# Kernel tuning notes

Hardware: AMD Instinct MI355X
Metric: run time of the kernel (lower is better)

Reference implementation:

```python
import jax, jax.numpy as jnp
import numpy as np

LAYERS, BLOCKS = 10, 3
N_BLK = LAYERS * BLOCKS
RC, SC, K = 128, 128, 2
IN_CH, COND_CH, OUT_CH = 256, 80, 256
DILATIONS = tuple(2 ** (i % LAYERS) for i in range(N_BLK))
INV_SQRT2 = 0.70710678118


def conv1x1(x, w, b):
    # x: [B, I, T], w: [O, I], b: [O] -> [B, O, T]
    return jnp.einsum('oi,bit->bot', w, x) + b[None, :, None]


def causal_conv(x, w, b, dilation):
    # x: [B, C, T], w: [O, I, K]; left-pad by (K-1)*d == torch pad-both + right slice
    pad = (w.shape[2] - 1) * dilation
    y = jax.lax.conv_general_dilated(
        x, w, window_strides=(1,), padding=[(pad, 0)],
        rhs_dilation=(dilation,), dimension_numbers=('NCH', 'OIH', 'NCH'))
    return y + b[None, :, None]


def setup_inputs() -> dict:
    key = jax.random.key(0)
    ks = jax.random.split(key, 20)
    s = 0.05
    B, T = 2, 8000
    inp = {
        'x': jax.random.normal(ks[0], (B, IN_CH, T), jnp.float32),
        'condition': jax.random.normal(ks[1], (B, COND_CH, T), jnp.float32),
        'input_w': jax.random.normal(ks[2], (RC, IN_CH), jnp.float32) * s,
        'input_b': jax.random.normal(ks[3], (RC,), jnp.float32) * s,
        'dil_w': jax.random.normal(ks[4], (N_BLK, RC, RC, K), jnp.float32) * s,
        'dil_b': jax.random.normal(ks[5], (N_BLK, RC), jnp.float32) * s,
        'gate_w': jax.random.normal(ks[6], (N_BLK, RC, RC), jnp.float32) * s,
        'gate_b': jax.random.normal(ks[7], (N_BLK, RC), jnp.float32) * s,
        'cond_w': jax.random.normal(ks[8], (N_BLK, RC, COND_CH), jnp.float32) * s,
        'cond_b': jax.random.normal(ks[9], (N_BLK, RC), jnp.float32) * s,
        'condg_w': jax.random.normal(ks[10], (N_BLK, RC, COND_CH), jnp.float32) * s,
        'condg_b': jax.random.normal(ks[11], (N_BLK, RC), jnp.float32) * s,
        'res_w': jax.random.normal(ks[12], (N_BLK, RC, RC), jnp.float32) * s,
        'res_b': jax.random.normal(ks[13], (N_BLK, RC), jnp.float32) * s,
        'skip_w': jax.random.normal(ks[14], (N_BLK, SC, RC), jnp.float32) * s,
        'skip_b': jax.random.normal(ks[15], (N_BLK, SC), jnp.float32) * s,
        'out1_w': jax.random.normal(ks[16], (SC, SC), jnp.float32) * s,
        'out1_b': jax.random.normal(ks[17], (SC,), jnp.float32) * s,
        'out2_w': jax.random.normal(ks[18], (OUT_CH, SC), jnp.float32) * s,
        'out2_b': jax.random.normal(ks[19], (OUT_CH,), jnp.float32) * s,
    }
    return inp


def reference(x, condition, input_w, input_b, dil_w, dil_b, gate_w, gate_b,
              cond_w, cond_b, condg_w, condg_b, res_w, res_b,
              skip_w, skip_b, out1_w, out1_b, out2_w, out2_b):
    h = conv1x1(x, input_w, input_b)  # [B, RC, T]
    skip = jnp.zeros_like(conv1x1(h, skip_w[0], skip_b[0]) * 0)  # [B, SC, T]
    for i, d in enumerate(DILATIONS):
        a = causal_conv(h, dil_w[i], dil_b[i], d) + conv1x1(condition, cond_w[i], cond_b[i])
        g = conv1x1(h, gate_w[i], gate_b[i]) + conv1x1(condition, condg_w[i], condg_b[i])
        out = jnp.tanh(a) * jax.nn.sigmoid(g)
        h = (h + conv1x1(out, res_w[i], res_b[i])) * INV_SQRT2
        skip = skip + conv1x1(out, skip_w[i], skip_b[i])
    y = jax.nn.relu(conv1x1(skip, out1_w, out1_b))
    return conv1x1(y, out2_w, out2_b)  # [B, 256, T]
```

## Files before the change

### kernel.cpp

```cpp
#include <hip/hip_runtime.h>

#define T_LEN 8000
#define NTPB 125
#define NBLK 250
#define NLAYER 30
#define GUARD 512
#define HROWS (GUARD + T_LEN)
#define SLAB (HROWS * 128)
#define INV_SQRT2 0.70710678118f

typedef short bf16x8 __attribute__((ext_vector_type(8)));
typedef unsigned uint2v __attribute__((ext_vector_type(2)));
typedef unsigned uint4v __attribute__((ext_vector_type(4)));
typedef float f32x4 __attribute__((ext_vector_type(4)));

#define R_HT  0
#define R_OUT 8192
#define R_CND 16384
#define WBASE 22528
#define LDS_SHORTS 71680

#define KLINE 4096
#define LS 106496
#define C1 16384
#define C2 32768
#define C3 49152
#define C4 57344
#define C5 73728
#define C6 90112
#define IN_OFF   3194880
#define OUT1_OFF 3227648
#define OUT2_OFF 3244032

#define WAITV(N) asm volatile("s_waitcnt vmcnt(" #N ")" ::: "memory")
#define LGKM0    asm volatile("s_waitcnt lgkmcnt(0)" ::: "memory")
#define BAR      asm volatile("s_barrier" ::: "memory")

__device__ __forceinline__ unsigned short f2bf_u(float f) {
    union { float f; unsigned u; } v; v.f = f;
    unsigned u = v.u + 0x7FFFu + ((v.u >> 16) & 1u);
    return (unsigned short)(u >> 16);
}
__device__ __forceinline__ short f2bf(float f) { return (short)f2bf_u(f); }

__device__ __forceinline__ unsigned cvtpk(float lo, float hi) {
    unsigned r;
    asm("v_cvt_pk_bf16_f32 %0, %1, %2" : "=v"(r) : "v"(lo), "v"(hi));
    return r;
}

__device__ __forceinline__ float gated_act(float av, float gv) {
    float e  = __expf(-2.f * fabsf(av));
    float th = (1.f - e) * __builtin_amdgcn_rcpf(1.f + e);
    th = (av < 0.f) ? -th : th;
    float sg = __builtin_amdgcn_rcpf(1.f + __expf(-gv));
    return th * sg;
}

__device__ __forceinline__ void ldg16_sc1(bf16x8* d, const short* p) {
    asm volatile("global_load_dwordx4 %0, %1, off sc1" : "=v"(*d) : "v"(p));
}
__device__ __forceinline__ void stg8_sc1(short* p, uint2v v) {
    asm volatile("global_store_dwordx2 %0, %1, off sc1" : : "v"(p), "v"(v) : "memory");
}
__device__ __forceinline__ void st_flag(int* p, int v) {
    __hip_atomic_store(p, v, __ATOMIC_RELAXED, __HIP_MEMORY_SCOPE_AGENT);
}
__device__ __forceinline__ void wait_ge(const int* p, int v) {
    while (__hip_atomic_load(p, __ATOMIC_RELAXED, __HIP_MEMORY_SCOPE_AGENT) < v)
        __builtin_amdgcn_s_sleep(1);
}

__device__ __forceinline__ f32x4 mfma_(bf16x8 a, bf16x8 b, f32x4 c) {
    return __builtin_amdgcn_mfma_f32_16x16x32_bf16(a, b, c, 0, 0, 0);
}

__device__ __forceinline__ void gload_lds16(const short* g, short* l) {
    __builtin_amdgcn_global_load_lds(
        (const __attribute__((address_space(1))) unsigned int*)g,
        (__attribute__((address_space(3))) unsigned int*)l, 16, 0, 0);
}
__device__ __forceinline__ void stageW2(const short* src, short* dst, int wv, int lane) {
    gload_lds16(src + wv * 512 + lane * 8, dst + wv * 512);
    gload_lds16(src + (16 + wv) * 512 + lane * 8, dst + (16 + wv) * 512);
}
__device__ __forceinline__ void stageW1(const short* src, short* dst, int wv, int lane) {
    gload_lds16(src + wv * 512 + lane * 8, dst + wv * 512);
}

template<int NP>
__device__ __forceinline__ void pairN(const short* wb, const short* sm, int boff,
                                      int ks0, int lg, int awoff,
                                      f32x4* ac0, f32x4* ac1)
{
#pragma unroll
    for (int p = 0; p < NP; ++p) {
        bf16x8 B = *(const bf16x8*)&sm[boff + ((ks0 + p) * 4 + lg) * 512];
#pragma unroll
        for (int mt = 0; mt < 2; ++mt) {
            bf16x8 a0 = *(const bf16x8*)&wb[p * 8192 + awoff + mt * 512];
            ac0[mt] = mfma_(a0, B, ac0[mt]);
            bf16x8 a1 = *(const bf16x8*)&wb[p * 8192 + 4096 + awoff + mt * 512];
            ac1[mt] = mfma_(a1, B, ac1[mt]);
        }
    }
}
template<int NP>
__device__ __forceinline__ void singleN(const short* wb, const short* sm, int boff,
                                        int ks0, int lg, int awoff, f32x4* ac)
{
#pragma unroll
    for (int p = 0; p < NP; ++p) {
        bf16x8 B = *(const bf16x8*)&sm[boff + ((ks0 + p) * 4 + lg) * 512];
#pragma unroll
        for (int mt = 0; mt < 2; ++mt) {
            bf16x8 a = *(const bf16x8*)&wb[p * 4096 + awoff + mt * 512];
            ac[mt] = mfma_(a, B, ac[mt]);
        }
    }
}

__global__ __launch_bounds__(256) void k_pack(
    const float* __restrict__ dil_w, const float* __restrict__ gate_w,
    const float* __restrict__ cond_w, const float* __restrict__ condg_w,
    const float* __restrict__ res_w, const float* __restrict__ skip_w,
    const float* __restrict__ input_w, const float* __restrict__ out1_w,
    const float* __restrict__ out2_w,
    const float* __restrict__ dil_b, const float* __restrict__ cond_b,
    const float* __restrict__ gate_b, const float* __restrict__ condg_b,
    short* __restrict__ wp, short* __restrict__ hbt, int* __restrict__ flg)
{
    int gid = blockIdx.x * 256 + threadIdx.x;
    if (gid < 512) flg[gid] = 0;
    {
        int g2 = gid - 512;
        if (g2 >= 0 && g2 < 262144) {
            unsigned* hb32 = (unsigned*)hbt;
            int slab = g2 >> 15, off = g2 & 32767;
            hb32[(size_t)slab * (SLAB / 2) + off] = 0u;
        }
    }
    if (gid >= 6400 * 64) return;
    int fid = gid >> 6, lane = gid & 63;
    int lr = lane & 15, lg = lane >> 4;
    float v[8];
    if (fid < 6240) {
        int layer = fid / 208;
        int r = fid - layer * 208;
        int kl = r >> 3, f = r & 7;
        int m = f * 16 + lr;
        size_t mi = (size_t)layer * 128 + m;
        int mat, ks;
        if      (kl < 8)  { mat = (kl & 1) ? 2 : 1; ks = kl >> 1; }
        else if (kl < 14) { mat = (kl & 1) ? 4 : 3; ks = (kl - 8) >> 1; }
        else if (kl < 18) { mat = 0; ks = kl - 14; }
        else              { mat = (kl & 1) ? 6 : 5; ks = (kl - 18) >> 1; }
        int kb = ks * 32 + lg * 8;
#pragma unroll
        for (int e = 0; e < 8; ++e) {
            int k = kb + e;
            float val;
            switch (mat) {
                case 0:  val = dil_w[(mi * 128 + k) * 2];     break;
                case 1:  val = dil_w[(mi * 128 + k) * 2 + 1]; break;
                case 2:  val = gate_w[mi * 128 + k]; break;
                case 3:  val = (k < 80) ? cond_w[mi * 80 + k]
                               : ((k == 80) ? dil_b[mi] + cond_b[mi] : 0.f); break;
                case 4:  val = (k < 80) ? condg_w[mi * 80 + k]
                               : ((k == 80) ? gate_b[mi] + condg_b[mi] : 0.f); break;
                case 5:  val = res_w[mi * 128 + k]; break;
                default: val = skip_w[mi * 128 + k]; break;
            }
            v[e] = val;
        }
    } else if (fid < 6304) {
        int f = fid - 6240; int ks = f >> 3, fr = f & 7;
        int m = fr * 16 + lr; int kb = ks * 32 + lg * 8;
#pragma unroll
        for (int e = 0; e < 8; ++e) v[e] = input_w[(size_t)m * 256 + kb + e];
    } else if (fid < 6336) {
        int f = fid - 6304; int ks = f >> 3, fr = f & 7;
        int m = fr * 16 + lr; int kb = ks * 32 + lg * 8;
#pragma unroll
        for (int e = 0; e < 8; ++e) v[e] = out1_w[(size_t)m * 128 + kb + e];
    } else {
        int f = fid - 6336; int mt = f & 15; int ks = f >> 4;
        int m = mt * 16 + lr; int kb = ks * 32 + lg * 8;
#pragma unroll
        for (int e = 0; e < 8; ++e) v[e] = out2_w[(size_t)m * 128 + kb + e];
    }
    short* dst = wp + (size_t)fid * 512 + lane * 8;
#pragma unroll
    for (int e = 0; e < 8; ++e) dst[e] = f2bf(v[e]);
}

__global__ __launch_bounds__(1024, 4) void k_wavenet(
    const float* __restrict__ x, const float* __restrict__ cond,
    const short* __restrict__ wp, short* __restrict__ hbt,
    const float* __restrict__ ib, const float* __restrict__ rbias,
    const float* __restrict__ sbias, const float* __restrict__ b1,
    const float* __restrict__ b2, float* __restrict__ outp,
    int* __restrict__ rdy, int* __restrict__ dn)
{
    __shared__ __align__(16) short sm[LDS_SHORTS];

    const int tid  = threadIdx.x;
    const int lane = tid & 63;
    const int wv   = __builtin_amdgcn_readfirstlane(tid >> 6);
    const int wm   = wv & 3;
    const int wn   = wv >> 2;
    const int lr   = lane & 15, lg = lane >> 4;
    const int bidx = blockIdx.x;
    const int b    = bidx / NTPB;
    const int ti   = bidx - b * NTPB;
    const int t0   = ti * 64;
    const int tl   = wn * 16 + lr;
    const int tg   = t0 + tl;
    const int tl8  = tl * 8;
    const int lane8 = lane * 8;
    const int awoff = wm * 1024 + lane8;
    const int chA  = wm * 32 + lg * 4;
    const int kbA  = wm * 4 + (lg >> 1);
    const int e0   = (lg & 1) * 4;

    stageW2(wp + IN_OFF, (short*)&sm[WBASE], wv, lane);
    stageW2(wp + IN_OFF + 16384, (short*)&sm[WBASE + 16384], wv, lane);
    {
        const float* xb = x + (size_t)b * 256 * T_LEN + t0 + lane;
#pragma unroll
        for (int it = 0; it < 2; ++it) {
            int kb = wv * 2 + it;
            unsigned pk[4];
#pragma unroll
            for (int e = 0; e < 4; ++e)
                pk[e] = cvtpk(xb[(size_t)(kb * 8 + 2 * e) * T_LEN],
                              xb[(size_t)(kb * 8 + 2 * e + 1) * T_LEN]);
            *(uint4v*)&sm[(kb * 64 + lane) * 8] = *(uint4v*)pk;
        }
        if (wv < 12) {
            const float* cb = cond + (size_t)b * 80 * T_LEN + t0 + lane;
            unsigned pk[4];
#pragma unroll
            for (int e = 0; e < 4; ++e) {
                int c0 = wv * 8 + 2 * e, c1 = c0 + 1;
                float v0 = (c0 < 80) ? cb[(size_t)c0 * T_LEN] : ((c0 == 80) ? 1.f : 0.f);
                float v1 = (c1 < 80) ? cb[(size_t)c1 * T_LEN] : 0.f;
                pk[e] = cvtpk(v0, v1);
            }
            *(uint4v*)&sm[R_CND + (wv * 64 + lane) * 8] = *(uint4v*)pk;
        }
    }
    __syncthreads();

    f32x4 hres[2] = {{0.f,0.f,0.f,0.f},{0.f,0.f,0.f,0.f}};
    {
        f32x4 acc[2] = {{0.f,0.f,0.f,0.f},{0.f,0.f,0.f,0.f}};
        singleN<4>((const short*)&sm[WBASE], sm, tl8, 0, lg, awoff, acc);
        singleN<4>((const short*)&sm[WBASE + 16384], sm, tl8, 4, lg, awoff, acc);
#pragma unroll
        for (int mt = 0; mt < 2; ++mt) {
            int cb0 = chA + mt * 16;
            f32x4 bv = {ib[cb0], ib[cb0 + 1], ib[cb0 + 2], ib[cb0 + 3]};
            hres[mt] = acc[mt] + bv;
        }
    }
    __syncthreads();
    {
        short* hrow = hbt + (size_t)b * SLAB + (size_t)(GUARD + tg) * 128 + chA;
#pragma unroll
        for (int mt = 0; mt < 2; ++mt) {
            uint2v hv = {cvtpk(hres[mt][0], hres[mt][1]), cvtpk(hres[mt][2], hres[mt][3])};
            stg8_sc1(hrow + mt * 16, hv);
            *(uint2v*)&sm[R_HT + ((kbA + mt * 2) * 64 + tl) * 8 + e0] = hv;
        }
    }
    asm volatile("s_waitcnt vmcnt(0)" ::: "memory");
    __syncthreads();
    if (tid == 0) st_flag(&rdy[bidx], 1);

    f32x4 skp[2] = {{0.f,0.f,0.f,0.f},{0.f,0.f,0.f,0.f}};

    int rot = 0;
    for (int li = 0; li < NLAYER; ++li) {
        const int d   = 1 << (li % 10);
        const int ksh = (d + 63) >> 6;
        const short* wl  = wp + (size_t)li * LS;
        const short* hcb = hbt + (size_t)((li & 3) * 2 + b) * SLAB;
        short*       hnb = hbt + (size_t)(((li + 1) & 3) * 2 + b) * SLAB;
        const int rA = rot;
        const int rB = (rot + 1) % 3;
        const int rC = (rot + 2) % 3;
        short* const sA = (short*)&sm[WBASE + rA * 16384];
        short* const sB = (short*)&sm[WBASE + rB * 16384];
        short* const sC = (short*)&sm[WBASE + rC * 16384];

        if (lane == 0 && ti >= ksh) wait_ge(&rdy[bidx - ksh], li + 1);

        f32x4 rbv[2], sbv[2];
        {
            const float* rbl = rbias + li * 128 + chA;
            const float* sbl = sbias + li * 128 + chA;
#pragma unroll
            for (int mt = 0; mt < 2; ++mt) {
                rbv[mt] = (f32x4){rbl[mt*16], rbl[mt*16+1], rbl[mt*16+2], rbl[mt*16+3]};
                sbv[mt] = (f32x4){sbl[mt*16], sbl[mt*16+1], sbl[mt*16+2], sbl[mt*16+3]};
            }
        }

        stageW2(wl, sA, wv, lane);
        bf16x8 Bg[4];
        {
            const short* hr = hcb + (size_t)(GUARD + tg - d) * 128 + lg * 8;
#pragma unroll
            for (int ks = 0; ks < 4; ++ks) ldg16_sc1(&Bg[ks], hr + ks * 32);
        }
        stageW2(wl + C1, sB, wv, lane);
        stageW2(wl + C2, sC, wv, lane);

        WAITV(8); BAR;
        f32x4 aa[2] = {{0.f,0.f,0.f,0.f},{0.f,0.f,0.f,0.f}};
        f32x4 ag[2] = {{0.f,0.f,0.f,0.f},{0.f,0.f,0.f,0.f}};
        pairN<2>(sA, sm, R_HT + tl8, 0, lg, awoff, aa, ag);

        WAITV(2); BAR;
        if (tid == 0) st_flag(&dn[bidx], li + 1);
        stageW1(wl + C3, sA, wv, lane);
        pairN<2>(sB, sm, R_HT + tl8, 2, lg, awoff, aa, ag);

        WAITV(1); BAR;
        stageW2(wl + C4, sB, wv, lane);
        pairN<2>(sC, sm, R_CND + tl8, 0, lg, awoff, aa, ag);

        WAITV(2); BAR;
        stageW2(wl + C5, sC, wv, lane);
        pairN<1>(sA, sm, R_CND + tl8, 2, lg, awoff, aa, ag);

        WAITV(2); BAR;
        stageW2(wl + C6, sA, wv, lane);
        {
#pragma unroll
            for (int ks = 0; ks < 4; ++ks) {
#pragma unroll
                for (int mt = 0; mt < 2; ++mt) {
                    bf16x8 a = *(const bf16x8*)&sB[ks * 4096 + awoff + mt * 512];
                    aa[mt] = mfma_(a, Bg[ks], aa[mt]);
                }
            }
        }
#pragma unroll
        for (int mt = 0; mt < 2; ++mt) {
            uint2v ov = {cvtpk(gated_act(aa[mt][0], ag[mt][0]), gated_act(aa[mt][1], ag[mt][1])),
                         cvtpk(gated_act(aa[mt][2], ag[mt][2]), gated_act(aa[mt][3], ag[mt][3]))};
            *(uint2v*)&sm[R_OUT + ((kbA + mt * 2) * 64 + tl) * 8 + e0] = ov;
        }
        WAITV(2); LGKM0; BAR;

        f32x4 ar[2]  = {{0.f,0.f,0.f,0.f},{0.f,0.f,0.f,0.f}};
        f32x4 as2[2] = {{0.f,0.f,0.f,0.f},{0.f,0.f,0.f,0.f}};
        pairN<2>(sC, sm, R_OUT + tl8, 0, lg, awoff, ar, as2);
        if (lane == 0 && li >= 3) {
            int d3 = 1 << ((li - 3) % 10);
            int k3 = (d3 + 63) >> 6;
            if (ti + k3 < NTPB) wait_ge(&dn[bidx + k3], li - 2);
        }
        WAITV(0); BAR;
        pairN<2>(sA, sm, R_OUT + tl8, 2, lg, awoff, ar, as2);

#pragma unroll
        for (int mt = 0; mt < 2; ++mt) {
            skp[mt]  = skp[mt] + as2[mt] + sbv[mt];
            hres[mt] = (hres[mt] + ar[mt] + rbv[mt]) * INV_SQRT2;
        }
        if (li < NLAYER - 1) {
            short* hrow = hnb + (size_t)(GUARD + tg) * 128 + chA;
#pragma unroll
            for (int mt = 0; mt < 2; ++mt) {
                uint2v hv = {cvtpk(hres[mt][0], hres[mt][1]), cvtpk(hres[mt][2], hres[mt][3])};
                stg8_sc1(hrow + mt * 16, hv);
                *(uint2v*)&sm[R_HT + ((kbA + mt * 2) * 64 + tl) * 8 + e0] = hv;
            }
        }
        WAITV(0); LGKM0; BAR;
        if (tid == 0 && li < NLAYER - 1) st_flag(&rdy[bidx], li + 2);
        rot = (rot + 1) % 3;
    }

    stageW2(wp + OUT1_OFF, (short*)&sm[WBASE], wv, lane);
    stageW2(wp + OUT2_OFF, (short*)&sm[WBASE + 16384], wv, lane);
    stageW2(wp + OUT2_OFF + 16384, (short*)&sm[WBASE + 32768], wv, lane);
#pragma unroll
    for (int mt = 0; mt < 2; ++mt) {
        uint2v sv = {cvtpk(skp[mt][0], skp[mt][1]), cvtpk(skp[mt][2], skp[mt][3])};
        *(uint2v*)&sm[R_HT + ((kbA + mt * 2) * 64 + tl) * 8 + e0] = sv;
    }
    __syncthreads();
    f32x4 ay[2] = {{0.f,0.f,0.f,0.f},{0.f,0.f,0.f,0.f}};
    singleN<4>((const short*)&sm[WBASE], sm, R_HT + tl8, 0, lg, awoff, ay);
#pragma unroll
    for (int mt = 0; mt < 2; ++mt) {
        int cb0 = chA + mt * 16;
        float y0 = fmaxf(ay[mt][0] + b1[cb0],     0.f);
        float y1 = fmaxf(ay[mt][1] + b1[cb0 + 1], 0.f);
        float y2 = fmaxf(ay[mt][2] + b1[cb0 + 2], 0.f);
        float y3 = fmaxf(ay[mt][3] + b1[cb0 + 3], 0.f);
        uint2v yv = {cvtpk(y0, y1), cvtpk(y2, y3)};
        *(uint2v*)&sm[R_OUT + ((kbA + mt * 2) * 64 + tl) * 8 + e0] = yv;
    }
    __syncthreads();
    f32x4 ao[4] = {{0.f,0.f,0.f,0.f},{0.f,0.f,0.f,0.f},
                   {0.f,0.f,0.f,0.f},{0.f,0.f,0.f,0.f}};
    {
        const short* w2a = (const short*)&sm[WBASE + 16384];
        const short* w2b = (const short*)&sm[WBASE + 32768];
#pragma unroll
        for (int ksp = 0; ksp < 2; ++ksp) {
            bf16x8 B = *(const bf16x8*)&sm[R_OUT + tl8 + (ksp * 4 + lg) * 512];
#pragma unroll
            for (int mt = 0; mt < 4; ++mt) {
                int fg = 4 * wm + mt;
                bf16x8 A = *(const bf16x8*)&w2a[(ksp * 2 + (fg >> 3)) * 4096 + (fg & 7) * 512 + lane8];
                ao[mt] = mfma_(A, B, ao[mt]);
            }
        }
#pragma unroll
        for (int ksp = 0; ksp < 2; ++ksp) {
            bf16x8 B = *(const bf16x8*)&sm[R_OUT + tl8 + ((2 + ksp) * 4 + lg) * 512];
#pragma unroll
            for (int mt = 0; mt < 4; ++mt) {
                int fg = 4 * wm + mt;
                bf16x8 A = *(const bf16x8*)&w2b[(ksp * 2 + (fg >> 3)) * 4096 + (fg & 7) * 512 + lane8];
                ao[mt] = mfma_(A, B, ao[mt]);
            }
        }
    }
#pragma unroll
    for (int mt = 0; mt < 4; ++mt) {
        int ch2 = wm * 64 + mt * 16 + lg * 4;
        float* op = outp + ((size_t)(b * 256 + ch2)) * T_LEN + tg;
        op[0]         = ao[mt][0] + b2[ch2];
        op[T_LEN]     = ao[mt][1] + b2[ch2 + 1];
        op[2 * T_LEN] = ao[mt][2] + b2[ch2 + 2];
        op[3 * T_LEN] = ao[mt][3] + b2[ch2 + 3];
    }
}

extern "C" void kernel_launch(void* const* d_in, const int* in_sizes, int n_in,
                              void* d_out, int out_size, void* d_ws, size_t ws_size,
                              hipStream_t stream)
{
    const float* x       = (const float*)d_in[0];
    const float* cond    = (const float*)d_in[1];
    const float* input_w = (const float*)d_in[2];
    const float* input_b = (const float*)d_in[3];
    const float* dil_w   = (const float*)d_in[4];
    const float* dil_b   = (const float*)d_in[5];
    const float* gate_w  = (const float*)d_in[6];
    const float* gate_b  = (const float*)d_in[7];
    const float* cond_w  = (const float*)d_in[8];
    const float* cond_b  = (const float*)d_in[9];
    const float* condg_w = (const float*)d_in[10];
    const float* condg_b = (const float*)d_in[11];
    const float* res_w   = (const float*)d_in[12];
    const float* res_b   = (const float*)d_in[13];
    const float* skip_w  = (const float*)d_in[14];
    const float* skip_b  = (const float*)d_in[15];
    const float* out1_w  = (const float*)d_in[16];
    const float* out1_b  = (const float*)d_in[17];
    const float* out2_w  = (const float*)d_in[18];
    const float* out2_b  = (const float*)d_in[19];
    float* outp = (float*)d_out;

    short* wpk = (short*)d_ws;
    short* hbt = wpk + (size_t)6400 * 512;
    int*   flg = (int*)(hbt + (size_t)8 * SLAB);
    int*   rdy = flg;
    int*   dn  = flg + 256;

    k_pack<<<1600, 256, 0, stream>>>(dil_w, gate_w, cond_w, condg_w, res_w, skip_w,
                                     input_w, out1_w, out2_w,
                                     dil_b, cond_b, gate_b, condg_b, wpk, hbt, flg);

    void* args[] = {(void*)&x, (void*)&cond, (void*)&wpk, (void*)&hbt,
                    (void*)&input_b, (void*)&res_b, (void*)&skip_b,
                    (void*)&out1_b, (void*)&out2_b, (void*)&outp,
                    (void*)&rdy, (void*)&dn};
    (void)hipLaunchCooperativeKernel((void*)k_wavenet, dim3(NBLK), dim3(1024), args, 0, stream);
}
```

Measured before the change: 328.4 us.

## Warp-specialize producer/consumer waves and deepen the h-buffer ring

Splits the 16 waves into 8 consumer waves that run all MFMA work (each handling two time sub-tiles) and 8 producer waves that stage weights into LDS and fetch the dilated h tile into a new LDS region. The ring of h buffers grows from 4 to 6 levels, and the global h layout changes from row-major with a guard to tiled slabs. This relaxes the cross-block dn dependency and moves the flag waits onto producer waves. The aim is to overlap global loads and inter-block waits with compute and cut the consumers' exposed latency. In exchange, compute is concentrated on half the waves, LDS use grows, and workspace footprint increases.

```diff
diff --git a/kernel.cpp b/kernel.cpp
--- a/kernel.cpp
+++ b/kernel.cpp
@@ -4,12 +4,14 @@
 #define NTPB 125
 #define NBLK 250
 #define NLAYER 30
-#define GUARD 512
-#define HROWS (GUARD + T_LEN)
-#define SLAB (HROWS * 128)
+#define NLVL 6
+#define GTILES 8
+#define TILES_ALL (GTILES + NTPB)
+#define SLAB ((size_t)TILES_ALL * 8192)
 #define INV_SQRT2 0.70710678118f
 
 typedef short bf16x8 __attribute__((ext_vector_type(8)));
+typedef short s16x4  __attribute__((ext_vector_type(4)));
 typedef unsigned uint2v __attribute__((ext_vector_type(2)));
 typedef unsigned uint4v __attribute__((ext_vector_type(4)));
 typedef float f32x4 __attribute__((ext_vector_type(4)));
@@ -17,10 +19,10 @@
 #define R_HT  0
 #define R_OUT 8192
 #define R_CND 16384
-#define WBASE 22528
-#define LDS_SHORTS 71680
-
-#define KLINE 4096
+#define R_HD  22528
+#define WBASE 30720
+#define LDS_SHORTS 79872
+
 #define LS 106496
 #define C1 16384
 #define C2 32768
@@ -42,13 +44,15 @@
     return (unsigned short)(u >> 16);
 }
 __device__ __forceinline__ short f2bf(float f) { return (short)f2bf_u(f); }
-
+__device__ __forceinline__ float bf2f(short s) {
+    union { unsigned u; float f; } v; v.u = ((unsigned)(unsigned short)s) << 16;
+    return v.f;
+}
 __device__ __forceinline__ unsigned cvtpk(float lo, float hi) {
     unsigned r;
     asm("v_cvt_pk_bf16_f32 %0, %1, %2" : "=v"(r) : "v"(lo), "v"(hi));
     return r;
 }
-
 __device__ __forceinline__ float gated_act(float av, float gv) {
     float e  = __expf(-2.f * fabsf(av));
     float th = (1.f - e) * __builtin_amdgcn_rcpf(1.f + e);
@@ -56,7 +60,6 @@
     float sg = __builtin_amdgcn_rcpf(1.f + __expf(-gv));
     return th * sg;
 }
-
 __device__ __forceinline__ void ldg16_sc1(bf16x8* d, const short* p) {
     asm volatile("global_load_dwordx4 %0, %1, off sc1" : "=v"(*d) : "v"(p));
 }
@@ -70,11 +73,9 @@
     while (__hip_atomic_load(p, __ATOMIC_RELAXED, __HIP_MEMORY_SCOPE_AGENT) < v)
         __builtin_amdgcn_s_sleep(1);
 }
-
 __device__ __forceinline__ f32x4 mfma_(bf16x8 a, bf16x8 b, f32x4 c) {
     return __builtin_amdgcn_mfma_f32_16x16x32_bf16(a, b, c, 0, 0, 0);
 }
-
 __device__ __forceinline__ void gload_lds16(const short* g, short* l) {
     __builtin_amdgcn_global_load_lds(
         (const __attribute__((address_space(1))) unsigned int*)g,
@@ -84,24 +85,56 @@
     gload_lds16(src + wv * 512 + lane * 8, dst + wv * 512);
     gload_lds16(src + (16 + wv) * 512 + lane * 8, dst + (16 + wv) * 512);
 }
-__device__ __forceinline__ void stageW1(const short* src, short* dst, int wv, int lane) {
-    gload_lds16(src + wv * 512 + lane * 8, dst + wv * 512);
+__device__ __forceinline__ void stageP4(const short* src, short* dst, int pv, int lane) {
+#pragma unroll
+    for (int r = 0; r < 4; ++r) {
+        int o = (r * 8 + pv) * 64;
+        gload_lds16(src + (o + lane) * 8, dst + o * 8);
+    }
+}
+__device__ __forceinline__ void stageP2(const short* src, short* dst, int pv, int lane) {
+#pragma unroll
+    for (int r = 0; r < 2; ++r) {
+        int o = (r * 8 + pv) * 64;
+        gload_lds16(src + (o + lane) * 8, dst + o * 8);
+    }
 }
 
 template<int NP>
-__device__ __forceinline__ void pairN(const short* wb, const short* sm, int boff,
-                                      int ks0, int lg, int awoff,
-                                      f32x4* ac0, f32x4* ac1)
+__device__ __forceinline__ void pair2t(const short* wb, const short* sm, int reg,
+                                       int tc0, int tc1, int ks0, int lg, int awoff,
+                                       f32x4 (&A)[2][2], f32x4 (&G)[2][2])
 {
 #pragma unroll
     for (int p = 0; p < NP; ++p) {
-        bf16x8 B = *(const bf16x8*)&sm[boff + ((ks0 + p) * 4 + lg) * 512];
+        int slot = reg + ((ks0 + p) * 4 + lg) * 512;
+        bf16x8 B0 = *(const bf16x8*)&sm[slot + tc0 * 8];
+        bf16x8 B1 = *(const bf16x8*)&sm[slot + tc1 * 8];
 #pragma unroll
         for (int mt = 0; mt < 2; ++mt) {
             bf16x8 a0 = *(const bf16x8*)&wb[p * 8192 + awoff + mt * 512];
-            ac0[mt] = mfma_(a0, B, ac0[mt]);
+            A[mt][0] = mfma_(a0, B0, A[mt][0]);
+            A[mt][1] = mfma_(a0, B1, A[mt][1]);
             bf16x8 a1 = *(const bf16x8*)&wb[p * 8192 + 4096 + awoff + mt * 512];
-            ac1[mt] = mfma_(a1, B, ac1[mt]);
+            G[mt][0] = mfma_(a1, B0, G[mt][0]);
+            G[mt][1] = mfma_(a1, B1, G[mt][1]);
+        }
+    }
+}
+__device__ __forceinline__ void d0gemm(const short* wb, const short* sm, int reg,
+                                       int tc0, int tc1, int lg, int awoff,
+                                       f32x4 (&A)[2][2])
+{
+#pragma unroll
+    for (int ks = 0; ks < 4; ++ks) {
+        int slot = reg + (ks * 4 + lg) * 512;
+        bf16x8 B0 = *(const bf16x8*)&sm[slot + tc0 * 8];
+        bf16x8 B1 = *(const bf16x8*)&sm[slot + tc1 * 8];
+#pragma unroll
+        for (int mt = 0; mt < 2; ++mt) {
+            bf16x8 a = *(const bf16x8*)&wb[ks * 4096 + awoff + mt * 512];
+            A[mt][0] = mfma_(a, B0, A[mt][0]);
+            A[mt][1] = mfma_(a, B1, A[mt][1]);
         }
     }
 }
@@ -134,7 +167,7 @@
     if (gid < 512) flg[gid] = 0;
     {
         int g2 = gid - 512;
-        if (g2 >= 0 && g2 < 262144) {
+        if (g2 >= 0 && g2 < 393216) {
             unsigned* hb32 = (unsigned*)hbt;
             int slab = g2 >> 15, off = g2 & 32767;
             hb32[(size_t)slab * (SLAB / 2) + off] = 0u;
@@ -208,23 +241,34 @@
     const int lane = tid & 63;
     const int wv   = __builtin_amdgcn_readfirstlane(tid >> 6);
     const int wm   = wv & 3;
-    const int wn   = wv >> 2;
+    const int wn4  = wv >> 2;
     const int lr   = lane & 15, lg = lane >> 4;
     const int bidx = blockIdx.x;
     const int b    = bidx / NTPB;
     const int ti   = bidx - b * NTPB;
     const int t0   = ti * 64;
-    const int tl   = wn * 16 + lr;
-    const int tg   = t0 + tl;
-    const int tl8  = tl * 8;
+    const int tl4  = wn4 * 16 + lr;
+    const int tg4  = t0 + tl4;
+    const int tl8  = tl4 * 8;
     const int lane8 = lane * 8;
     const int awoff = wm * 1024 + lane8;
     const int chA  = wm * 32 + lg * 4;
     const int kbA  = wm * 4 + (lg >> 1);
     const int e0   = (lg & 1) * 4;
-
-    stageW2(wp + IN_OFF, (short*)&sm[WBASE], wv, lane);
-    stageW2(wp + IN_OFF + 16384, (short*)&sm[WBASE + 16384], wv, lane);
+    const bool cons = (wv < 8);
+    const int pv   = wv - 8;
+    const int wn2  = wn4 & 1;
+    const int tc0  = wn2 * 32 + lr;
+    const int tc1  = tc0 + 16;
+    const int tgc0 = t0 + tc0;
+    const int tgc1 = t0 + tc1;
+
+    short* const sA = (short*)&sm[WBASE];
+    short* const sB = (short*)&sm[WBASE + 16384];
+    short* const sC = (short*)&sm[WBASE + 32768];
+
+    stageW2(wp + IN_OFF, sA, wv, lane);
+    stageW2(wp + IN_OFF + 16384, sB, wv, lane);
     {
         const float* xb = x + (size_t)b * 256 * T_LEN + t0 + lane;
 #pragma unroll
@@ -252,52 +296,47 @@
     }
     __syncthreads();
 
-    f32x4 hres[2] = {{0.f,0.f,0.f,0.f},{0.f,0.f,0.f,0.f}};
     {
         f32x4 acc[2] = {{0.f,0.f,0.f,0.f},{0.f,0.f,0.f,0.f}};
-        singleN<4>((const short*)&sm[WBASE], sm, tl8, 0, lg, awoff, acc);
-        singleN<4>((const short*)&sm[WBASE + 16384], sm, tl8, 4, lg, awoff, acc);
+        singleN<4>(sA, sm, tl8, 0, lg, awoff, acc);
+        singleN<4>(sB, sm, tl8, 4, lg, awoff, acc);
+        __syncthreads();
+        short* h0t = hbt + (size_t)(0 * 2 + b) * SLAB + (size_t)(ti + GTILES) * 8192;
 #pragma unroll
         for (int mt = 0; mt < 2; ++mt) {
             int cb0 = chA + mt * 16;
-            f32x4 bv = {ib[cb0], ib[cb0 + 1], ib[cb0 + 2], ib[cb0 + 3]};
-            hres[mt] = acc[mt] + bv;
-        }
-    }
-    __syncthreads();
-    {
-        short* hrow = hbt + (size_t)b * SLAB + (size_t)(GUARD + tg) * 128 + chA;
-#pragma unroll
-        for (int mt = 0; mt < 2; ++mt) {
-            uint2v hv = {cvtpk(hres[mt][0], hres[mt][1]), cvtpk(hres[mt][2], hres[mt][3])};
-            stg8_sc1(hrow + mt * 16, hv);
-            *(uint2v*)&sm[R_HT + ((kbA + mt * 2) * 64 + tl) * 8 + e0] = hv;
-        }
-    }
-    asm volatile("s_waitcnt vmcnt(0)" ::: "memory");
+            f32x4 hv = acc[mt] + (f32x4){ib[cb0], ib[cb0+1], ib[cb0+2], ib[cb0+3]};
+            uint2v pk = {cvtpk(hv[0], hv[1]), cvtpk(hv[2], hv[3])};
+            stg8_sc1(h0t + (kbA + mt * 2) * 512 + tl4 * 8 + e0, pk);
+            *(uint2v*)&sm[R_HT + ((kbA + mt * 2) * 64 + tl4) * 8 + e0] = pk;
+        }
+    }
+    WAITV(0); LGKM0;
     __syncthreads();
     if (tid == 0) st_flag(&rdy[bidx], 1);
 
-    f32x4 skp[2] = {{0.f,0.f,0.f,0.f},{0.f,0.f,0.f,0.f}};
-
-    int rot = 0;
+    f32x4 hres[2][2], skp[2][2];
+    if (cons) {
+#pragma unroll
+        for (int mt = 0; mt < 2; ++mt) {
+            s16x4 h0 = *(const s16x4*)&sm[R_HT + ((kbA + mt*2) * 64 + tc0) * 8 + e0];
+            s16x4 h1 = *(const s16x4*)&sm[R_HT + ((kbA + mt*2) * 64 + tc1) * 8 + e0];
+            hres[mt][0] = (f32x4){bf2f(h0[0]), bf2f(h0[1]), bf2f(h0[2]), bf2f(h0[3])};
+            hres[mt][1] = (f32x4){bf2f(h1[0]), bf2f(h1[1]), bf2f(h1[2]), bf2f(h1[3])};
+            skp[mt][0] = (f32x4){0.f,0.f,0.f,0.f};
+            skp[mt][1] = (f32x4){0.f,0.f,0.f,0.f};
+        }
+    }
+
     for (int li = 0; li < NLAYER; ++li) {
         const int d   = 1 << (li % 10);
         const int ksh = (d + 63) >> 6;
         const short* wl  = wp + (size_t)li * LS;
-        const short* hcb = hbt + (size_t)((li & 3) * 2 + b) * SLAB;
-        short*       hnb = hbt + (size_t)(((li + 1) & 3) * 2 + b) * SLAB;
-        const int rA = rot;
-        const int rB = (rot + 1) % 3;
-        const int rC = (rot + 2) % 3;
-        short* const sA = (short*)&sm[WBASE + rA * 16384];
-        short* const sB = (short*)&sm[WBASE + rB * 16384];
-        short* const sC = (short*)&sm[WBASE + rC * 16384];
-
-        if (lane == 0 && ti >= ksh) wait_ge(&rdy[bidx - ksh], li + 1);
+        const short* hcb = hbt + (size_t)((li % NLVL) * 2 + b) * SLAB;
+        short*       hnb = hbt + (size_t)(((li + 1) % NLVL) * 2 + b) * SLAB;
 
         f32x4 rbv[2], sbv[2];
-        {
+        if (cons) {
             const float* rbl = rbias + li * 128 + chA;
             const float* sbl = sbias + li * 128 + chA;
 #pragma unroll
@@ -305,97 +344,127 @@
                 rbv[mt] = (f32x4){rbl[mt*16], rbl[mt*16+1], rbl[mt*16+2], rbl[mt*16+3]};
                 sbv[mt] = (f32x4){sbl[mt*16], sbl[mt*16+1], sbl[mt*16+2], sbl[mt*16+3]};
             }
-        }
-
-        stageW2(wl, sA, wv, lane);
-        bf16x8 Bg[4];
-        {
-            const short* hr = hcb + (size_t)(GUARD + tg - d) * 128 + lg * 8;
-#pragma unroll
-            for (int ks = 0; ks < 4; ++ks) ldg16_sc1(&Bg[ks], hr + ks * 32);
-        }
-        stageW2(wl + C1, sB, wv, lane);
-        stageW2(wl + C2, sC, wv, lane);
-
-        WAITV(8); BAR;
-        f32x4 aa[2] = {{0.f,0.f,0.f,0.f},{0.f,0.f,0.f,0.f}};
-        f32x4 ag[2] = {{0.f,0.f,0.f,0.f},{0.f,0.f,0.f,0.f}};
-        pairN<2>(sA, sm, R_HT + tl8, 0, lg, awoff, aa, ag);
-
-        WAITV(2); BAR;
-        if (tid == 0) st_flag(&dn[bidx], li + 1);
-        stageW1(wl + C3, sA, wv, lane);
-        pairN<2>(sB, sm, R_HT + tl8, 2, lg, awoff, aa, ag);
-
-        WAITV(1); BAR;
-        stageW2(wl + C4, sB, wv, lane);
-        pairN<2>(sC, sm, R_CND + tl8, 0, lg, awoff, aa, ag);
-
-        WAITV(2); BAR;
-        stageW2(wl + C5, sC, wv, lane);
-        pairN<1>(sA, sm, R_CND + tl8, 2, lg, awoff, aa, ag);
-
-        WAITV(2); BAR;
-        stageW2(wl + C6, sA, wv, lane);
-        {
-#pragma unroll
-            for (int ks = 0; ks < 4; ++ks) {
+        } else {
+            stageP4(wl,      sA, pv, lane);
+            stageP4(wl + C1, sB, pv, lane);
+            stageP4(wl + C2, sC, pv, lane);
+            if (pv == 0 && lane == 0 && ti >= ksh)
+                wait_ge(&rdy[bidx - ksh], li + 1);
+            if (pv == 1 && lane == 0 && li >= NLVL - 1) {
+                int d5 = 1 << ((li - (NLVL - 1)) % 10);
+                int k5 = (d5 + 63) >> 6;
+                if (ti + k5 < NTPB) wait_ge(&dn[bidx + k5], li - NLVL + 2);
+            }
+            WAITV(8);
+        }
+        BAR;
+        f32x4 aa[2][2], ag[2][2];
+        if (cons) {
+#pragma unroll
+            for (int mt = 0; mt < 2; ++mt) {
+                aa[mt][0] = (f32x4){0.f,0.f,0.f,0.f}; aa[mt][1] = (f32x4){0.f,0.f,0.f,0.f};
+                ag[mt][0] = (f32x4){0.f,0.f,0.f,0.f}; ag[mt][1] = (f32x4){0.f,0.f,0.f,0.f};
+            }
+            pair2t<2>(sA, sm, R_HT, tc0, tc1, 0, lg, awoff, aa, ag);
+        } else {
+            bf16x8 bh0, bh1;
+            int kb0 = pv * 2;
+            int gg = t0 - d + lane + GTILES * 64;
+            const short* s0 = hcb + (size_t)(gg >> 6) * 8192 + kb0 * 512 + (gg & 63) * 8;
+            ldg16_sc1(&bh0, s0);
+            ldg16_sc1(&bh1, s0 + 512);
+            WAITV(0);
+            __builtin_amdgcn_sched_barrier(0);
+            *(bf16x8*)&sm[R_HD + kb0 * 512 + lane8] = bh0;
+            *(bf16x8*)&sm[R_HD + (kb0 + 1) * 512 + lane8] = bh1;
+            LGKM0;
+        }
+        BAR;
+        if (cons) pair2t<2>(sB, sm, R_HT, tc0, tc1, 2, lg, awoff, aa, ag);
+        else      stageP2(wl + C3, sA, pv, lane);
+        BAR;
+        if (cons) pair2t<2>(sC, sm, R_CND, tc0, tc1, 0, lg, awoff, aa, ag);
+        else    { stageP4(wl + C4, sB, pv, lane); WAITV(4); }
+        BAR;
+        if (cons) pair2t<1>(sA, sm, R_CND, tc0, tc1, 2, lg, awoff, aa, ag);
+        else    { stageP4(wl + C5, sC, pv, lane); WAITV(4); }
+        BAR;
+        if (cons) {
+            d0gemm(sB, sm, R_HD, tc0, tc1, lg, awoff, aa);
+#pragma unroll
+            for (int mt = 0; mt < 2; ++mt) {
+                uint2v o0 = {cvtpk(gated_act(aa[mt][0][0], ag[mt][0][0]),
+                                   gated_act(aa[mt][0][1], ag[mt][0][1])),
+                             cvtpk(gated_act(aa[mt][0][2], ag[mt][0][2]),
+                                   gated_act(aa[mt][0][3], ag[mt][0][3]))};
+                uint2v o1 = {cvtpk(gated_act(aa[mt][1][0], ag[mt][1][0]),
+                                   gated_act(aa[mt][1][1], ag[mt][1][1])),
+                             cvtpk(gated_act(aa[mt][1][2], ag[mt][1][2]),
+                                   gated_act(aa[mt][1][3], ag[mt][1][3]))};
+                *(uint2v*)&sm[R_OUT + ((kbA + mt*2) * 64 + tc0) * 8 + e0] = o0;
+                *(uint2v*)&sm[R_OUT + ((kbA + mt*2) * 64 + tc1) * 8 + e0] = o1;
+            }
+            LGKM0;
+        } else { stageP4(wl + C6, sA, pv, lane); WAITV(4); }
+        BAR;
+        if (cons && wv == 0 && lane == 0) st_flag(&dn[bidx], li + 1);
+        f32x4 ar[2][2], as2[2][2];
+        if (cons) {
+#pragma unroll
+            for (int mt = 0; mt < 2; ++mt) {
+                ar[mt][0] = (f32x4){0.f,0.f,0.f,0.f}; ar[mt][1] = (f32x4){0.f,0.f,0.f,0.f};
+                as2[mt][0] = (f32x4){0.f,0.f,0.f,0.f}; as2[mt][1] = (f32x4){0.f,0.f,0.f,0.f};
+            }
+            pair2t<2>(sC, sm, R_OUT, tc0, tc1, 0, lg, awoff, ar, as2);
+        } else {
+            WAITV(0);
+        }
+        BAR;
+        if (cons) {
+            pair2t<2>(sA, sm, R_OUT, tc0, tc1, 2, lg, awoff, ar, as2);
+#pragma unroll
+            for (int mt = 0; mt < 2; ++mt) {
+                hres[mt][0] = (hres[mt][0] + ar[mt][0] + rbv[mt]) * INV_SQRT2;
+                hres[mt][1] = (hres[mt][1] + ar[mt][1] + rbv[mt]) * INV_SQRT2;
+                skp[mt][0] = skp[mt][0] + as2[mt][0] + sbv[mt];
+                skp[mt][1] = skp[mt][1] + as2[mt][1] + sbv[mt];
+            }
+            if (li < NLAYER - 1) {
+                short* hti = hnb + (size_t)(ti + GTILES) * 8192;
 #pragma unroll
                 for (int mt = 0; mt < 2; ++mt) {
-                    bf16x8 a = *(const bf16x8*)&sB[ks * 4096 + awoff + mt * 512];
-                    aa[mt] = mfma_(a, Bg[ks], aa[mt]);
+                    uint2v h0 = {cvtpk(hres[mt][0][0], hres[mt][0][1]),
+                                 cvtpk(hres[mt][0][2], hres[mt][0][3])};
+                    uint2v h1 = {cvtpk(hres[mt][1][0], hres[mt][1][1]),
+                                 cvtpk(hres[mt][1][2], hres[mt][1][3])};
+                    stg8_sc1(hti + (kbA + mt*2) * 512 + tc0 * 8 + e0, h0);
+                    stg8_sc1(hti + (kbA + mt*2) * 512 + tc1 * 8 + e0, h1);
+                    *(uint2v*)&sm[R_HT + ((kbA + mt*2) * 64 + tc0) * 8 + e0] = h0;
+                    *(uint2v*)&sm[R_HT + ((kbA + mt*2) * 64 + tc1) * 8 + e0] = h1;
                 }
             }
-        }
+            WAITV(0); LGKM0;
+        }
+        BAR;
+        if (cons && wv == 0 && lane == 0 && li < NLAYER - 1)
+            st_flag(&rdy[bidx], li + 2);
+    }
+
+    if (cons) {
 #pragma unroll
         for (int mt = 0; mt < 2; ++mt) {
-            uint2v ov = {cvtpk(gated_act(aa[mt][0], ag[mt][0]), gated_act(aa[mt][1], ag[mt][1])),
-                         cvtpk(gated_act(aa[mt][2], ag[mt][2]), gated_act(aa[mt][3], ag[mt][3]))};
-            *(uint2v*)&sm[R_OUT + ((kbA + mt * 2) * 64 + tl) * 8 + e0] = ov;
-        }
-        WAITV(2); LGKM0; BAR;
-
-        f32x4 ar[2]  = {{0.f,0.f,0.f,0.f},{0.f,0.f,0.f,0.f}};
-        f32x4 as2[2] = {{0.f,0.f,0.f,0.f},{0.f,0.f,0.f,0.f}};
-        pairN<2>(sC, sm, R_OUT + tl8, 0, lg, awoff, ar, as2);
-        if (lane == 0 && li >= 3) {
-            int d3 = 1 << ((li - 3) % 10);
-            int k3 = (d3 + 63) >> 6;
-            if (ti + k3 < NTPB) wait_ge(&dn[bidx + k3], li - 2);
-        }
-        WAITV(0); BAR;
-        pairN<2>(sA, sm, R_OUT + tl8, 2, lg, awoff, ar, as2);
-
-#pragma unroll
-        for (int mt = 0; mt < 2; ++mt) {
-            skp[mt]  = skp[mt] + as2[mt] + sbv[mt];
-            hres[mt] = (hres[mt] + ar[mt] + rbv[mt]) * INV_SQRT2;
-        }
-        if (li < NLAYER - 1) {
-            short* hrow = hnb + (size_t)(GUARD + tg) * 128 + chA;
-#pragma unroll
-            for (int mt = 0; mt < 2; ++mt) {
-                uint2v hv = {cvtpk(hres[mt][0], hres[mt][1]), cvtpk(hres[mt][2], hres[mt][3])};
-                stg8_sc1(hrow + mt * 16, hv);
-                *(uint2v*)&sm[R_HT + ((kbA + mt * 2) * 64 + tl) * 8 + e0] = hv;
-            }
-        }
-        WAITV(0); LGKM0; BAR;
-        if (tid == 0 && li < NLAYER - 1) st_flag(&rdy[bidx], li + 2);
-        rot = (rot + 1) % 3;
-    }
-
-    stageW2(wp + OUT1_OFF, (short*)&sm[WBASE], wv, lane);
-    stageW2(wp + OUT2_OFF, (short*)&sm[WBASE + 16384], wv, lane);
-    stageW2(wp + OUT2_OFF + 16384, (short*)&sm[WBASE + 32768], wv, lane);
-#pragma unroll
-    for (int mt = 0; mt < 2; ++mt) {
-        uint2v sv = {cvtpk(skp[mt][0], skp[mt][1]), cvtpk(skp[mt][2], skp[mt][3])};
-        *(uint2v*)&sm[R_HT + ((kbA + mt * 2) * 64 + tl) * 8 + e0] = sv;
-    }
+            uint2v s0 = {cvtpk(skp[mt][0][0], skp[mt][0][1]), cvtpk(skp[mt][0][2], skp[mt][0][3])};
+            uint2v s1 = {cvtpk(skp[mt][1][0], skp[mt][1][1]), cvtpk(skp[mt][1][2], skp[mt][1][3])};
+            *(uint2v*)&sm[R_HT + ((kbA + mt*2) * 64 + tc0) * 8 + e0] = s0;
+            *(uint2v*)&sm[R_HT + ((kbA + mt*2) * 64 + tc1) * 8 + e0] = s1;
+        }
+    }
+    stageW2(wp + OUT1_OFF, sA, wv, lane);
+    stageW2(wp + OUT2_OFF, sB, wv, lane);
+    stageW2(wp + OUT2_OFF + 16384, sC, wv, lane);
     __syncthreads();
     f32x4 ay[2] = {{0.f,0.f,0.f,0.f},{0.f,0.f,0.f,0.f}};
-    singleN<4>((const short*)&sm[WBASE], sm, R_HT + tl8, 0, lg, awoff, ay);
+    singleN<4>(sA, sm, R_HT + tl8, 0, lg, awoff, ay);
 #pragma unroll
     for (int mt = 0; mt < 2; ++mt) {
         int cb0 = chA + mt * 16;
@@ -404,21 +473,19 @@
         float y2 = fmaxf(ay[mt][2] + b1[cb0 + 2], 0.f);
         float y3 = fmaxf(ay[mt][3] + b1[cb0 + 3], 0.f);
         uint2v yv = {cvtpk(y0, y1), cvtpk(y2, y3)};
-        *(uint2v*)&sm[R_OUT + ((kbA + mt * 2) * 64 + tl) * 8 + e0] = yv;
+        *(uint2v*)&sm[R_OUT + ((kbA + mt * 2) * 64 + tl4) * 8 + e0] = yv;
     }
     __syncthreads();
     f32x4 ao[4] = {{0.f,0.f,0.f,0.f},{0.f,0.f,0.f,0.f},
                    {0.f,0.f,0.f,0.f},{0.f,0.f,0.f,0.f}};
     {
-        const short* w2a = (const short*)&sm[WBASE + 16384];
-        const short* w2b = (const short*)&sm[WBASE + 32768];
 #pragma unroll
         for (int ksp = 0; ksp < 2; ++ksp) {
             bf16x8 B = *(const bf16x8*)&sm[R_OUT + tl8 + (ksp * 4 + lg) * 512];
 #pragma unroll
             for (int mt = 0; mt < 4; ++mt) {
                 int fg = 4 * wm + mt;
-                bf16x8 A = *(const bf16x8*)&w2a[(ksp * 2 + (fg >> 3)) * 4096 + (fg & 7) * 512 + lane8];
+                bf16x8 A = *(const bf16x8*)&sB[(ksp * 2 + (fg >> 3)) * 4096 + (fg & 7) * 512 + lane8];
                 ao[mt] = mfma_(A, B, ao[mt]);
             }
         }
@@ -428,7 +495,7 @@
 #pragma unroll
             for (int mt = 0; mt < 4; ++mt) {
                 int fg = 4 * wm + mt;
-                bf16x8 A = *(const bf16x8*)&w2b[(ksp * 2 + (fg >> 3)) * 4096 + (fg & 7) * 512 + lane8];
+                bf16x8 A = *(const bf16x8*)&sC[(ksp * 2 + (fg >> 3)) * 4096 + (fg & 7) * 512 + lane8];
                 ao[mt] = mfma_(A, B, ao[mt]);
             }
         }
@@ -436,7 +503,7 @@
 #pragma unroll
     for (int mt = 0; mt < 4; ++mt) {
         int ch2 = wm * 64 + mt * 16 + lg * 4;
-        float* op = outp + ((size_t)(b * 256 + ch2)) * T_LEN + tg;
+        float* op = outp + ((size_t)(b * 256 + ch2)) * T_LEN + tg4;
         op[0]         = ao[mt][0] + b2[ch2];
         op[T_LEN]     = ao[mt][1] + b2[ch2 + 1];
         op[2 * T_LEN] = ao[mt][2] + b2[ch2 + 2];
@@ -472,7 +539,7 @@
 
     short* wpk = (short*)d_ws;
     short* hbt = wpk + (size_t)6400 * 512;
-    int*   flg = (int*)(hbt + (size_t)8 * SLAB);
+    int*   flg = (int*)(hbt + (size_t)12 * SLAB);
     int*   rdy = flg;
     int*   dn  = flg + 256;
 
```

Result: slower. 559.6 us (+70.4%).
